# Performance work log

Hardware: AMD Instinct MI355X
Metric: run time of the kernel (lower is better)

## Reference

```python
import jax, jax.numpy as jnp
import numpy as np

HIDDEN = 5120
N_HEADS = 128
Q_LORA = 1536
KV_LORA = 512
ROPE_D = 64
NOPE_D = 128
V_D = 128
Q_HEAD_D = NOPE_D + ROPE_D  # 192
ROPE_BASE = 10000.0
EPS = 1e-6
B, QL, KVL = 32, 1, 4096


def rms_norm(x, w):
    var = jnp.mean(x.astype(jnp.float32) ** 2, axis=-1, keepdims=True)
    return (x.astype(jnp.float32) * jax.lax.rsqrt(var + EPS)).astype(x.dtype) * w


def rotate_half(x):
    x1, x2 = x[..., : x.shape[-1] // 2], x[..., x.shape[-1] // 2 :]
    return jnp.concatenate([-x2, x1], axis=-1)


def apply_rope(q, position_ids):
    # q: [b, h, s, d]; position_ids: [b, s]
    d = q.shape[-1]
    inv_freq = 1.0 / (ROPE_BASE ** (jnp.arange(0, d, 2, dtype=jnp.float32) / d))
    freqs = position_ids.astype(jnp.float32)[..., None] * inv_freq  # [b, s, d/2]
    emb = jnp.concatenate([freqs, freqs], axis=-1)                  # [b, s, d]
    cos = jnp.cos(emb)[:, None].astype(q.dtype)  # [b, 1, s, d]
    sin = jnp.sin(emb)[:, None].astype(q.dtype)
    # de-interleave: view(b,h,s,d//2,2).transpose(4,3).reshape == [even dims | odd dims]
    q = jnp.concatenate([q[..., 0::2], q[..., 1::2]], axis=-1)
    return q * cos + rotate_half(q) * sin


def setup_inputs() -> dict:
    key = jax.random.key(0)
    ks = jax.random.split(key, 8)
    w = 0.02  # keep activations in a sane range
    return {
        "hidden_states_q": jax.random.normal(ks[0], (B, QL, HIDDEN), jnp.float32),
        "q_position_ids": jax.random.randint(ks[1], (B, QL), 0, 4096, jnp.int64) if jax.config.read('jax_enable_x64') else jax.random.randint(ks[1], (B, QL), 0, 4096, jnp.int32),
        "compressed_kv": jax.random.normal(ks[2], (B, KVL, KV_LORA + ROPE_D), jnp.float32),
        "Wq_a": jax.random.normal(ks[3], (Q_LORA, HIDDEN), jnp.float32) * w,
        "q_a_ln_w": jnp.ones((Q_LORA,), jnp.float32),
        "Wq_b": jax.random.normal(ks[4], (N_HEADS * Q_HEAD_D, Q_LORA), jnp.float32) * w,
        "Wkv_b": jax.random.normal(ks[5], (N_HEADS * (NOPE_D + V_D), KV_LORA), jnp.float32) * w,
        "Wo": jax.random.normal(ks[6], (HIDDEN, N_HEADS * V_D), jnp.float32) * w,
    }


def reference(hidden_states_q, q_position_ids, compressed_kv, Wq_a, q_a_ln_w, Wq_b, Wkv_b, Wo):
    b, q_len, _ = hidden_states_q.shape
    # low-rank query path
    q_a = hidden_states_q @ Wq_a.T                      # [b, q, q_lora]
    q = rms_norm(q_a, q_a_ln_w) @ Wq_b.T                # [b, q, h*192]
    q = q.reshape(b, q_len, N_HEADS, Q_HEAD_D).transpose(0, 2, 1, 3)  # [b, h, q, 192]
    q_nope, q_pe = q[..., :NOPE_D], q[..., NOPE_D:]

    ckv = compressed_kv[..., :KV_LORA]                  # [b, kv, 512] (values/latent keys)
    # absorbed projections from kv_b weight
    kv_b = Wkv_b.reshape(N_HEADS, NOPE_D + V_D, KV_LORA)
    q_absorb = kv_b[:, :NOPE_D, :]                      # [h, 128, 512]
    out_absorb = kv_b[:, NOPE_D:, :]                    # [h, 128, 512]

    q_pe = apply_rope(q_pe, q_position_ids)             # [b, h, q, 64]
    q_lat = jnp.einsum('hdc,bhqd->bhqc', q_absorb, q_nope)  # [b, h, q, 512]
    query = jnp.concatenate([q_lat, q_pe], axis=-1)     # [b, h, q, 576]

    scale = 1.0 / np.sqrt(Q_HEAD_D).astype(np.float32)
    scores = jnp.einsum('bhqc,bkc->bhqk', query, compressed_kv) * scale  # [b, h, q, kv]
    probs = jax.nn.softmax(scores, axis=-1)
    attn = jnp.einsum('bhqk,bkc->bhqc', probs, ckv)     # [b, h, q, 512]
    o = jnp.einsum('bhqc,hvc->bhqv', attn, out_absorb)  # [b, h, q, 128]
    o = o.transpose(0, 2, 1, 3).reshape(b, q_len, N_HEADS * V_D)
    return o @ Wo.T                                     # [b, q, hidden]
```

## Files before the change

### kernel.cpp

```cpp
#include <hip/hip_runtime.h>
#include <stdint.h>

#define NHEADS 128
#define QLORA 1536
#define QHD 192
#define NOPED 128
#define BB 32
#define KVL 4096
#define CKVD 576

typedef __attribute__((ext_vector_type(8))) short short8;
typedef __attribute__((ext_vector_type(4))) float f32x4;

union FragU {
  uint4 u4;
  unsigned u[4];
  short8 s8;
};

__device__ inline unsigned short f2bf(float x){
  unsigned u = __float_as_uint(x);
  u += 0x7FFFu + ((u>>16)&1u);
  return (unsigned short)(u>>16);
}
__device__ inline float bf2f(unsigned short h){ return __uint_as_float(((unsigned)h)<<16); }
__device__ inline unsigned pk2(float lo, float hi){
  return (unsigned)f2bf(lo) | ((unsigned)f2bf(hi)<<16);
}

__device__ inline FragU load8(const float* p){
  float4 a = *(const float4*)p;
  float4 b = *(const float4*)(p+4);
  FragU f;
  f.u[0] = pk2(a.x,a.y); f.u[1] = pk2(a.z,a.w);
  f.u[2] = pk2(b.x,b.y); f.u[3] = pk2(b.z,b.w);
  return f;
}
__device__ inline FragU load8(const unsigned short* p){
  FragU f; f.u4 = *(const uint4*)p; return f;
}

__device__ inline f32x4 MFMA(const FragU& a, const FragU& b, f32x4 c){
  return __builtin_amdgcn_mfma_f32_16x16x32_bf16(a.s8, b.s8, c, 0, 0, 0);
}

__global__ void k_detect(const unsigned* lnw, const unsigned* pos, int* flags){
  if (threadIdx.x == 0){
    flags[0] = (lnw[0] == 0x3F803F80u) ? 1 : 0;
    unsigned o = 0;
    for (int i=0;i<8;i++) o |= pos[2*i+1];
    flags[1] = (o == 0u) ? 1 : 0;
  }
}

struct GP {
  int xstr, xzoff;
  int wstr; long wzoff, woff0;
  int cstr; long czoff;
  int kchunk, ksteps;
};

template<typename TX, typename TW, bool ATOMIC>
__device__ inline void gemm_body(const TX* __restrict__ X, const TW* __restrict__ W,
                                 float* __restrict__ C, GP g){
  const int tid = threadIdx.x;
  const int w = tid>>6, l = tid&63, quad = l>>4, m = l&15;
  const int z = blockIdx.z;
  const int n0 = (blockIdx.x*4 + w)*16;
  const int k0 = blockIdx.y * g.kchunk;
  const TX* xp0 = X + (size_t)z*g.xzoff + (size_t)m*g.xstr + k0 + quad*8;
  const TX* xp1 = xp0 + (size_t)16*g.xstr;
  const TW* wp  = W + g.woff0 + (size_t)z*g.wzoff + (size_t)(n0+m)*g.wstr + k0 + quad*8;
  f32x4 acc0 = {0.f,0.f,0.f,0.f};
  f32x4 acc1 = {0.f,0.f,0.f,0.f};
  for (int ks=0; ks<g.ksteps; ks++){
    FragU a0 = load8(xp0);
    FragU a1 = load8(xp1);
    FragU bb = load8(wp);
    acc0 = MFMA(a0, bb, acc0);
    acc1 = MFMA(a1, bb, acc1);
    xp0 += 32; xp1 += 32; wp += 32;
  }
  float* cp = C + (size_t)z*g.czoff + (n0 + m);
  #pragma unroll
  for (int r=0;r<4;r++){
    int row0 = quad*4 + r;
    if (ATOMIC){
      atomicAdd(cp + (size_t)row0*g.cstr, acc0[r]);
      atomicAdd(cp + (size_t)(row0+16)*g.cstr, acc1[r]);
    } else {
      cp[(size_t)row0*g.cstr] = acc0[r];
      cp[(size_t)(row0+16)*g.cstr] = acc1[r];
    }
  }
}

template<int XT, int WT, bool ATOMIC>
__global__ __launch_bounds__(256) void k_gemm(const void* X, const void* W, float* C,
                                              GP g, const int* flags){
  if constexpr (XT==2 && WT==2){
    if (flags[0]) gemm_body<unsigned short, unsigned short, ATOMIC>((const unsigned short*)X,(const unsigned short*)W,C,g);
    else          gemm_body<float, float, ATOMIC>((const float*)X,(const float*)W,C,g);
  } else if constexpr (XT==0 && WT==2){
    if (flags[0]) gemm_body<float, unsigned short, ATOMIC>((const float*)X,(const unsigned short*)W,C,g);
    else          gemm_body<float, float, ATOMIC>((const float*)X,(const float*)W,C,g);
  } else {
    gemm_body<float, unsigned short, ATOMIC>((const float*)X,(const unsigned short*)W,C,g);
  }
}

__global__ __launch_bounds__(256) void k_rms(const float* qa, const void* lnw, float* qn,
                                             const int* flags){
  int b = blockIdx.x, tid = threadIdx.x;
  __shared__ float red[4];
  float s = 0.f;
  for (int i=tid; i<QLORA; i+=256){ float v = qa[b*QLORA+i]; s += v*v; }
  for (int d=32; d; d>>=1) s += __shfl_down(s, d, 64);
  if ((tid&63)==0) red[tid>>6] = s;
  __syncthreads();
  float tot = red[0]+red[1]+red[2]+red[3];
  float rs = rsqrtf(tot/(float)QLORA + 1e-6f);
  bool bf = flags[0] != 0;
  for (int i=tid; i<QLORA; i+=256){
    float wv = bf ? bf2f(((const unsigned short*)lnw)[i]) : ((const float*)lnw)[i];
    qn[b*QLORA+i] = qa[b*QLORA+i]*rs*wv;
  }
}

__global__ __launch_bounds__(256) void k_transpose(const void* wkvb, unsigned short* qabsT,
                                                   const int* flags){
  int h = blockIdx.y, c0 = blockIdx.x*64, tid = threadIdx.x;
  __shared__ float t[128][65];
  bool bf = flags[0] != 0;
  for (int i=0;i<32;i++){
    int e = tid + i*256; int d = e>>6; int c = e&63;
    size_t idx = ((size_t)(h*256 + d))*512 + c0 + c;
    t[d][c] = bf ? bf2f(((const unsigned short*)wkvb)[idx]) : ((const float*)wkvb)[idx];
  }
  __syncthreads();
  for (int i=0;i<32;i++){
    int e = tid + i*256; int cc = e>>7; int d = e&127;
    qabsT[((size_t)h*512 + c0 + cc)*128 + d] = f2bf(t[d][cc]);
  }
}

__global__ void k_rope(const float* q, const void* posp, float* query, const int* flags){
  int idx = blockIdx.x*256 + threadIdx.x;
  if (idx >= BB*NHEADS) return;
  int b = idx>>7, h = idx&127;
  long p = flags[1] ? (long)((const long long*)posp)[b] : (long)((const int*)posp)[b];
  const float* qp = q + (size_t)b*(NHEADS*QHD) + h*QHD + NOPED;
  float* o = query + ((size_t)b*NHEADS + h)*CKVD + 512;
  for (int i=0;i<32;i++){
    double invf = pow(10000.0, -((double)(2*i))/64.0);
    double fr = (double)p * invf;
    double cs = cos(fr), sn = sin(fr);
    float q0 = qp[2*i], q1 = qp[2*i+1];
    o[i]      = (float)((double)q0*cs - (double)q1*sn);
    o[32 + i] = (float)((double)q1*cs + (double)q0*sn);
  }
}

#define KS 32
#define KROW 584
#define VROW 40

template<typename T> struct PFT;
template<> struct PFT<float>          { typedef float4 type; };
template<> struct PFT<unsigned short> { typedef uint2  type; };

__device__ inline void cv4(const float4& v, unsigned& d0, unsigned& d1){ d0 = pk2(v.x,v.y); d1 = pk2(v.z,v.w); }
__device__ inline void cv4(const uint2&  v, unsigned& d0, unsigned& d1){ d0 = v.x; d1 = v.y; }

template<typename TK>
__device__ inline void attn_body(const TK* __restrict__ ckv, const float* __restrict__ query,
                                 float* __restrict__ pacc, float* __restrict__ pml,
                                 int NC, int CH,
                                 unsigned short* sK, unsigned short* sV, unsigned short* sP){
  const int b = blockIdx.y, chunk = blockIdx.x;
  const int tid = threadIdx.x;
  const int w = tid>>6, l = tid&63, quad = l>>4, m = l&15;
  const int kbase = chunk*CH;
  const int nsub = CH/KS;
  const float SCALE = 0.07216878364870323f;
  const float L2E = 1.4426950408889634f;

  FragU qf[18];
  {
    const float* qrow = query + ((size_t)b*NHEADS + w*16 + m)*CKVD + quad*8;
    #pragma unroll
    for (int s=0;s<18;s++){
      float4 a = *(const float4*)(qrow + s*32);
      float4 c = *(const float4*)(qrow + s*32 + 4);
      qf[s].u[0] = pk2(a.x*SCALE, a.y*SCALE);
      qf[s].u[1] = pk2(a.z*SCALE, a.w*SCALE);
      qf[s].u[2] = pk2(c.x*SCALE, c.y*SCALE);
      qf[s].u[3] = pk2(c.z*SCALE, c.w*SCALE);
    }
  }

  f32x4 oacc[32];
  #pragma unroll
  for (int i=0;i<32;i++) oacc[i] = (f32x4){0.f,0.f,0.f,0.f};
  float M[4] = {-3e38f,-3e38f,-3e38f,-3e38f};
  float L[4] = {0.f,0.f,0.f,0.f};

  typedef typename PFT<TK>::type PT;
  PT pf[9];

  auto do_load = [&](int sc){
    const TK* base = ckv + ((size_t)b*KVL + kbase + sc*KS)*CKVD;
    #pragma unroll
    for (int i=0;i<9;i++){
      int u = i*512 + tid; int key = u&31; int c = (u>>5)<<2;
      pf[i] = *(const PT*)(base + (size_t)key*CKVD + c);
    }
  };
  auto stage_write = [&](){
    #pragma unroll
    for (int i=0;i<9;i++){
      int u = i*512 + tid; int key = u&31; int c = (u>>5)<<2;
      unsigned d0, d1; cv4(pf[i], d0, d1);
      *(uint2*)&sK[key*KROW + c] = make_uint2(d0, d1);
      if (c < 512){
        sV[(c+0)*VROW + key] = (unsigned short)(d0 & 0xffffu);
        sV[(c+1)*VROW + key] = (unsigned short)(d0 >> 16);
        sV[(c+2)*VROW + key] = (unsigned short)(d1 & 0xffffu);
        sV[(c+3)*VROW + key] = (unsigned short)(d1 >> 16);
      }
    }
  };
  auto compute = [&](){
    f32x4 s0 = {0.f,0.f,0.f,0.f};
    f32x4 s1 = {0.f,0.f,0.f,0.f};
    #pragma unroll
    for (int ks=0;ks<18;ks++){
      FragU b0, b1;
      b0.u4 = *(const uint4*)&sK[(size_t)m*KROW + ks*32 + quad*8];
      b1.u4 = *(const uint4*)&sK[(size_t)(m+16)*KROW + ks*32 + quad*8];
      s0 = MFMA(qf[ks], b0, s0);
      s1 = MFMA(qf[ks], b1, s1);
    }
    float al[4], p0[4], p1[4];
    #pragma unroll
    for (int r=0;r<4;r++){
      float mx = fmaxf(s0[r], s1[r]);
      for (int d=1; d<16; d<<=1) mx = fmaxf(mx, __shfl_xor(mx, d, 64));
      float nm = fmaxf(M[r], mx);
      al[r] = exp2f((M[r]-nm)*L2E);
      M[r] = nm;
      p0[r] = exp2f((s0[r]-nm)*L2E);
      p1[r] = exp2f((s1[r]-nm)*L2E);
      float sm = p0[r]+p1[r];
      for (int d=1; d<16; d<<=1) sm += __shfl_xor(sm, d, 64);
      L[r] = L[r]*al[r] + sm;
    }
    #pragma unroll
    for (int ct=0;ct<32;ct++){
      #pragma unroll
      for (int r=0;r<4;r++) oacc[ct][r] *= al[r];
    }
    #pragma unroll
    for (int r=0;r<4;r++){
      sP[(w*16 + quad*4 + r)*VROW + m]      = f2bf(p0[r]);
      sP[(w*16 + quad*4 + r)*VROW + 16 + m] = f2bf(p1[r]);
    }
    asm volatile("s_waitcnt lgkmcnt(0)" ::: "memory");
    FragU pa; pa.u4 = *(const uint4*)&sP[(w*16 + m)*VROW + quad*8];
    #pragma unroll
    for (int ct=0;ct<32;ct++){
      FragU vb; vb.u4 = *(const uint4*)&sV[(ct*16 + m)*VROW + quad*8];
      oacc[ct] = MFMA(pa, vb, oacc[ct]);
    }
  };

  do_load(0);
  for (int sc=0; sc<nsub; sc++){
    __syncthreads();
    stage_write();
    if (sc+1 < nsub) do_load(sc+1);
    __syncthreads();
    compute();
  }

  #pragma unroll
  for (int ct=0; ct<32; ct++){
    #pragma unroll
    for (int r=0;r<4;r++){
      int h = w*16 + quad*4 + r;
      size_t o = (((size_t)(b*NHEADS + h))*NC + chunk)*512 + ct*16 + m;
      pacc[o] = oacc[ct][r];
    }
  }
  if (m == 0){
    #pragma unroll
    for (int r=0;r<4;r++){
      int h = w*16 + quad*4 + r;
      size_t o = (((size_t)(b*NHEADS + h))*NC + chunk)*2;
      pml[o] = M[r]; pml[o+1] = L[r];
    }
  }
}

__global__ __launch_bounds__(512) void k_attn(const void* ckv, const float* query,
                                              float* pacc, float* pml, const int* flags,
                                              int NC, int CH){
  __shared__ __align__(16) unsigned short sK[KS*KROW];
  __shared__ __align__(16) unsigned short sV[512*VROW];
  __shared__ __align__(16) unsigned short sP[8*16*VROW];
  if (flags[0]) attn_body<unsigned short>((const unsigned short*)ckv, query, pacc, pml, NC, CH, sK, sV, sP);
  else          attn_body<float>((const float*)ckv, query, pacc, pml, NC, CH, sK, sV, sP);
}

__global__ __launch_bounds__(256) void k_reduce(const float* pacc, const float* pml,
                                                float* attn, int NC){
  int bh = blockIdx.x;
  int tid = threadIdx.x;
  float Ms[8], Ls[8];
  float Mg = -3e38f;
  for (int i=0;i<NC;i++){
    Ms[i] = pml[((size_t)bh*NC + i)*2];
    Ls[i] = pml[((size_t)bh*NC + i)*2 + 1];
    Mg = fmaxf(Mg, Ms[i]);
  }
  float f[8]; float tot = 0.f;
  for (int i=0;i<NC;i++){
    f[i] = exp2f((Ms[i]-Mg)*1.4426950408889634f);
    tot += f[i]*Ls[i];
  }
  float rc = 1.f/tot;
  for (int c=tid; c<512; c+=256){
    float s = 0.f;
    for (int i=0;i<NC;i++) s += f[i]*pacc[((size_t)bh*NC + i)*512 + c];
    attn[(size_t)bh*512 + c] = s*rc;
  }
}

__global__ void k_cast(const float* src, void* dst, const int* flags, int n){
  int i = blockIdx.x*256 + threadIdx.x;
  if (i < n){
    if (flags[0]) ((unsigned short*)dst)[i] = f2bf(src[i]);
    else          ((float*)dst)[i] = src[i];
  }
}

extern "C" void kernel_launch(void* const* d_in, const int* in_sizes, int n_in,
                              void* d_out, int out_size, void* d_ws, size_t ws_size,
                              hipStream_t stream){
  const void* hs   = d_in[0];
  const void* pos  = d_in[1];
  const void* ckv  = d_in[2];
  const void* wqa  = d_in[3];
  const void* lnw  = d_in[4];
  const void* wqb  = d_in[5];
  const void* wkvb = d_in[6];
  const void* wo   = d_in[7];

  char* ws = (char*)d_ws;
  size_t off = 0;
  auto alloc = [&](size_t bytes)->char*{
    char* p = ws + off;
    off = (off + bytes + 255) & ~(size_t)255;
    return p;
  };
  int* flags = (int*)alloc(16);
  char* zbase = ws + off;
  float* q_a   = (float*)alloc((size_t)32*1536*4);
  float* q     = (float*)alloc((size_t)32*24576*4);
  float* o_acc = (float*)alloc((size_t)32*5120*4);
  size_t zbytes = (size_t)((ws + off) - zbase);
  float* qn    = (float*)alloc((size_t)32*1536*4);
  float* query = (float*)alloc((size_t)32*128*576*4);
  unsigned short* qabsT = (unsigned short*)alloc((size_t)128*512*128*2);
  float* attn  = (float*)alloc((size_t)32*128*512*4);
  float* o     = (float*)alloc((size_t)32*16384*4);

  int NC = 8;
  while (NC > 1 && off + (size_t)32*128*NC*512*4 + (size_t)32*128*NC*2*4 + 1024 > ws_size) NC >>= 1;
  float* pacc = (float*)alloc((size_t)32*128*NC*512*4);
  float* pml  = (float*)alloc((size_t)32*128*NC*2*4);
  int CH = KVL/NC;

  (void)hipMemsetAsync(zbase, 0, zbytes, stream);
  hipLaunchKernelGGL(k_detect, dim3(1), dim3(64), 0, stream,
                     (const unsigned*)lnw, (const unsigned*)pos, flags);

  GP g;
  g = {}; g.xstr=5120; g.xzoff=0; g.wstr=5120; g.wzoff=0; g.woff0=0;
  g.cstr=1536; g.czoff=0; g.kchunk=640; g.ksteps=20;
  hipLaunchKernelGGL((k_gemm<2,2,true>), dim3(24,8,1), dim3(256), 0, stream, hs, wqa, q_a, g, flags);

  hipLaunchKernelGGL(k_rms, dim3(32), dim3(256), 0, stream, q_a, lnw, qn, flags);

  g = {}; g.xstr=1536; g.xzoff=0; g.wstr=1536; g.wzoff=0; g.woff0=0;
  g.cstr=24576; g.czoff=0; g.kchunk=384; g.ksteps=12;
  hipLaunchKernelGGL((k_gemm<0,2,true>), dim3(384,4,1), dim3(256), 0, stream, qn, wqb, q, g, flags);

  hipLaunchKernelGGL(k_transpose, dim3(8,128), dim3(256), 0, stream, wkvb, qabsT, flags);

  g = {}; g.xstr=24576; g.xzoff=192; g.wstr=128; g.wzoff=65536; g.woff0=0;
  g.cstr=128*576; g.czoff=576; g.kchunk=128; g.ksteps=4;
  hipLaunchKernelGGL((k_gemm<0,1,false>), dim3(8,1,128), dim3(256), 0, stream, q, qabsT, query, g, flags);

  hipLaunchKernelGGL(k_rope, dim3(16), dim3(256), 0, stream, q, pos, query, flags);

  hipLaunchKernelGGL(k_attn, dim3(NC,32), dim3(512), 0, stream, ckv, query, pacc, pml, flags, NC, CH);

  hipLaunchKernelGGL(k_reduce, dim3(32*128), dim3(256), 0, stream, pacc, pml, attn, NC);

  g = {}; g.xstr=128*512; g.xzoff=512; g.wstr=512; g.wzoff=131072; g.woff0=65536;
  g.cstr=16384; g.czoff=128; g.kchunk=512; g.ksteps=16;
  hipLaunchKernelGGL((k_gemm<0,2,false>), dim3(2,1,128), dim3(256), 0, stream, attn, wkvb, o, g, flags);

  g = {}; g.xstr=16384; g.xzoff=0; g.wstr=16384; g.wzoff=0; g.woff0=0;
  g.cstr=5120; g.czoff=0; g.kchunk=2048; g.ksteps=64;
  hipLaunchKernelGGL((k_gemm<0,2,true>), dim3(80,8,1), dim3(256), 0, stream, o, wo, o_acc, g, flags);

  hipLaunchKernelGGL(k_cast, dim3((32*5120+255)/256), dim3(256), 0, stream, o_acc, d_out, flags, 32*5120);
}
```

Measured before the change: 1.175 ms.

## Templatize GEMM k-steps, bf16 attention partials, float rope, attn occupancy hint

Makes the GEMM k-step count a template parameter and unrolls the loop by four, so loads can be issued earlier. Stores the per-chunk attention partial accumulators as bf16 instead of fp32 and vectorises the reduce kernel's reads, halving that intermediate traffic. Replaces the double-precision pow/cos/sin in rope with float powf/sincosf. Adds a min-blocks hint of 2 to the attention kernel's launch bounds, which can limit registers and risks spills. The bf16 partials and float rope both reduce numerical precision.

Result: faster. 1.127 ms (-4.1%).

```diff
diff --git a/kernel.cpp b/kernel.cpp
--- a/kernel.cpp
+++ b/kernel.cpp
@@ -57,10 +57,10 @@
   int xstr, xzoff;
   int wstr; long wzoff, woff0;
   int cstr; long czoff;
-  int kchunk, ksteps;
+  int kchunk;
 };
 
-template<typename TX, typename TW, bool ATOMIC>
+template<typename TX, typename TW, bool ATOMIC, int KSTEPS>
 __device__ inline void gemm_body(const TX* __restrict__ X, const TW* __restrict__ W,
                                  float* __restrict__ C, GP g){
   const int tid = threadIdx.x;
@@ -73,7 +73,8 @@
   const TW* wp  = W + g.woff0 + (size_t)z*g.wzoff + (size_t)(n0+m)*g.wstr + k0 + quad*8;
   f32x4 acc0 = {0.f,0.f,0.f,0.f};
   f32x4 acc1 = {0.f,0.f,0.f,0.f};
-  for (int ks=0; ks<g.ksteps; ks++){
+  #pragma unroll 4
+  for (int ks=0; ks<KSTEPS; ks++){
     FragU a0 = load8(xp0);
     FragU a1 = load8(xp1);
     FragU bb = load8(wp);
@@ -95,17 +96,17 @@
   }
 }
 
-template<int XT, int WT, bool ATOMIC>
+template<int XT, int WT, bool ATOMIC, int KSTEPS>
 __global__ __launch_bounds__(256) void k_gemm(const void* X, const void* W, float* C,
                                               GP g, const int* flags){
   if constexpr (XT==2 && WT==2){
-    if (flags[0]) gemm_body<unsigned short, unsigned short, ATOMIC>((const unsigned short*)X,(const unsigned short*)W,C,g);
-    else          gemm_body<float, float, ATOMIC>((const float*)X,(const float*)W,C,g);
+    if (flags[0]) gemm_body<unsigned short, unsigned short, ATOMIC, KSTEPS>((const unsigned short*)X,(const unsigned short*)W,C,g);
+    else          gemm_body<float, float, ATOMIC, KSTEPS>((const float*)X,(const float*)W,C,g);
   } else if constexpr (XT==0 && WT==2){
-    if (flags[0]) gemm_body<float, unsigned short, ATOMIC>((const float*)X,(const unsigned short*)W,C,g);
-    else          gemm_body<float, float, ATOMIC>((const float*)X,(const float*)W,C,g);
+    if (flags[0]) gemm_body<float, unsigned short, ATOMIC, KSTEPS>((const float*)X,(const unsigned short*)W,C,g);
+    else          gemm_body<float, float, ATOMIC, KSTEPS>((const float*)X,(const float*)W,C,g);
   } else {
-    gemm_body<float, unsigned short, ATOMIC>((const float*)X,(const unsigned short*)W,C,g);
+    gemm_body<float, unsigned short, ATOMIC, KSTEPS>((const float*)X,(const unsigned short*)W,C,g);
   }
 }
 
@@ -151,13 +152,15 @@
   long p = flags[1] ? (long)((const long long*)posp)[b] : (long)((const int*)posp)[b];
   const float* qp = q + (size_t)b*(NHEADS*QHD) + h*QHD + NOPED;
   float* o = query + ((size_t)b*NHEADS + h)*CKVD + 512;
+  float pf = (float)p;
   for (int i=0;i<32;i++){
-    double invf = pow(10000.0, -((double)(2*i))/64.0);
-    double fr = (double)p * invf;
-    double cs = cos(fr), sn = sin(fr);
+    float invf = powf(10000.0f, -((float)(2*i))/64.0f);
+    float fr = pf * invf;
+    float cs, sn;
+    sincosf(fr, &sn, &cs);
     float q0 = qp[2*i], q1 = qp[2*i+1];
-    o[i]      = (float)((double)q0*cs - (double)q1*sn);
-    o[32 + i] = (float)((double)q1*cs + (double)q0*sn);
+    o[i]      = q0*cs - q1*sn;
+    o[32 + i] = q1*cs + q0*sn;
   }
 }
 
@@ -174,7 +177,7 @@
 
 template<typename TK>
 __device__ inline void attn_body(const TK* __restrict__ ckv, const float* __restrict__ query,
-                                 float* __restrict__ pacc, float* __restrict__ pml,
+                                 unsigned short* __restrict__ pacc, float* __restrict__ pml,
                                  int NC, int CH,
                                  unsigned short* sK, unsigned short* sV, unsigned short* sP){
   const int b = blockIdx.y, chunk = blockIdx.x;
@@ -289,7 +292,7 @@
     for (int r=0;r<4;r++){
       int h = w*16 + quad*4 + r;
       size_t o = (((size_t)(b*NHEADS + h))*NC + chunk)*512 + ct*16 + m;
-      pacc[o] = oacc[ct][r];
+      pacc[o] = f2bf(oacc[ct][r]);
     }
   }
   if (m == 0){
@@ -302,9 +305,9 @@
   }
 }
 
-__global__ __launch_bounds__(512) void k_attn(const void* ckv, const float* query,
-                                              float* pacc, float* pml, const int* flags,
-                                              int NC, int CH){
+__global__ __launch_bounds__(512, 2) void k_attn(const void* ckv, const float* query,
+                                                 unsigned short* pacc, float* pml, const int* flags,
+                                                 int NC, int CH){
   __shared__ __align__(16) unsigned short sK[KS*KROW];
   __shared__ __align__(16) unsigned short sV[512*VROW];
   __shared__ __align__(16) unsigned short sP[8*16*VROW];
@@ -312,7 +315,7 @@
   else          attn_body<float>((const float*)ckv, query, pacc, pml, NC, CH, sK, sV, sP);
 }
 
-__global__ __launch_bounds__(256) void k_reduce(const float* pacc, const float* pml,
+__global__ __launch_bounds__(256) void k_reduce(const unsigned short* pacc, const float* pml,
                                                 float* attn, int NC){
   int bh = blockIdx.x;
   int tid = threadIdx.x;
@@ -329,11 +332,15 @@
     tot += f[i]*Ls[i];
   }
   float rc = 1.f/tot;
-  for (int c=tid; c<512; c+=256){
-    float s = 0.f;
-    for (int i=0;i<NC;i++) s += f[i]*pacc[((size_t)bh*NC + i)*512 + c];
-    attn[(size_t)bh*512 + c] = s*rc;
-  }
+  int c0 = tid*2;
+  float s0 = 0.f, s1 = 0.f;
+  for (int i=0;i<NC;i++){
+    unsigned v = *(const unsigned*)&pacc[((size_t)bh*NC + i)*512 + c0];
+    s0 += f[i]*bf2f((unsigned short)(v & 0xffffu));
+    s1 += f[i]*bf2f((unsigned short)(v >> 16));
+  }
+  attn[(size_t)bh*512 + c0]     = s0*rc;
+  attn[(size_t)bh*512 + c0 + 1] = s1*rc;
 }
 
 __global__ void k_cast(const float* src, void* dst, const int* flags, int n){
@@ -376,8 +383,8 @@
   float* o     = (float*)alloc((size_t)32*16384*4);
 
   int NC = 8;
-  while (NC > 1 && off + (size_t)32*128*NC*512*4 + (size_t)32*128*NC*2*4 + 1024 > ws_size) NC >>= 1;
-  float* pacc = (float*)alloc((size_t)32*128*NC*512*4);
+  while (NC > 1 && off + (size_t)32*128*NC*512*2 + (size_t)32*128*NC*2*4 + 1024 > ws_size) NC >>= 1;
+  unsigned short* pacc = (unsigned short*)alloc((size_t)32*128*NC*512*2);
   float* pml  = (float*)alloc((size_t)32*128*NC*2*4);
   int CH = KVL/NC;
 
@@ -387,20 +394,20 @@
 
   GP g;
   g = {}; g.xstr=5120; g.xzoff=0; g.wstr=5120; g.wzoff=0; g.woff0=0;
-  g.cstr=1536; g.czoff=0; g.kchunk=640; g.ksteps=20;
-  hipLaunchKernelGGL((k_gemm<2,2,true>), dim3(24,8,1), dim3(256), 0, stream, hs, wqa, q_a, g, flags);
+  g.cstr=1536; g.czoff=0; g.kchunk=640;
+  hipLaunchKernelGGL((k_gemm<2,2,true,20>), dim3(24,8,1), dim3(256), 0, stream, hs, wqa, q_a, g, flags);
 
   hipLaunchKernelGGL(k_rms, dim3(32), dim3(256), 0, stream, q_a, lnw, qn, flags);
 
   g = {}; g.xstr=1536; g.xzoff=0; g.wstr=1536; g.wzoff=0; g.woff0=0;
-  g.cstr=24576; g.czoff=0; g.kchunk=384; g.ksteps=12;
-  hipLaunchKernelGGL((k_gemm<0,2,true>), dim3(384,4,1), dim3(256), 0, stream, qn, wqb, q, g, flags);
+  g.cstr=24576; g.czoff=0; g.kchunk=384;
+  hipLaunchKernelGGL((k_gemm<0,2,true,12>), dim3(384,4,1), dim3(256), 0, stream, qn, wqb, q, g, flags);
 
   hipLaunchKernelGGL(k_transpose, dim3(8,128), dim3(256), 0, stream, wkvb, qabsT, flags);
 
   g = {}; g.xstr=24576; g.xzoff=192; g.wstr=128; g.wzoff=65536; g.woff0=0;
-  g.cstr=128*576; g.czoff=576; g.kchunk=128; g.ksteps=4;
-  hipLaunchKernelGGL((k_gemm<0,1,false>), dim3(8,1,128), dim3(256), 0, stream, q, qabsT, query, g, flags);
+  g.cstr=128*576; g.czoff=576; g.kchunk=128;
+  hipLaunchKernelGGL((k_gemm<0,1,false,4>), dim3(8,1,128), dim3(256), 0, stream, q, qabsT, query, g, flags);
 
   hipLaunchKernelGGL(k_rope, dim3(16), dim3(256), 0, stream, q, pos, query, flags);
 
@@ -409,12 +416,12 @@
   hipLaunchKernelGGL(k_reduce, dim3(32*128), dim3(256), 0, stream, pacc, pml, attn, NC);
 
   g = {}; g.xstr=128*512; g.xzoff=512; g.wstr=512; g.wzoff=131072; g.woff0=65536;
-  g.cstr=16384; g.czoff=128; g.kchunk=512; g.ksteps=16;
-  hipLaunchKernelGGL((k_gemm<0,2,false>), dim3(2,1,128), dim3(256), 0, stream, attn, wkvb, o, g, flags);
+  g.cstr=16384; g.czoff=128; g.kchunk=512;
+  hipLaunchKernelGGL((k_gemm<0,2,false,16>), dim3(2,1,128), dim3(256), 0, stream, attn, wkvb, o, g, flags);
 
   g = {}; g.xstr=16384; g.xzoff=0; g.wstr=16384; g.wzoff=0; g.woff0=0;
-  g.cstr=5120; g.czoff=0; g.kchunk=2048; g.ksteps=64;
-  hipLaunchKernelGGL((k_gemm<0,2,true>), dim3(80,8,1), dim3(256), 0, stream, o, wo, o_acc, g, flags);
+  g.cstr=5120; g.czoff=0; g.kchunk=2048;
+  hipLaunchKernelGGL((k_gemm<0,2,true,64>), dim3(80,8,1), dim3(256), 0, stream, o, wo, o_acc, g, flags);
 
   hipLaunchKernelGGL(k_cast, dim3((32*5120+255)/256), dim3(256), 0, stream, o_acc, d_out, flags, 32*5120);
 }
```
